# Kernel optimization log

Hardware: AMD Instinct MI355X
Metric: run time of the kernel (lower is better)

Reference implementation:

```python
import jax, jax.numpy as jnp
import numpy as np

# --- dimensions (match init_kwargs) ---
T, B = 64, 8            # time steps, batch
H, I, O, G = 512, 256, 8, 4   # hidden, input, output, attention groups
GS = I // G              # group size = 64 (equal groups)
E_H = int(0.8 * H)       # 409 excitatory hidden units
ZC = round(0.2 * H)      # 102 zeroed columns for h2o / attn masks
DT = 0.02
AX = DT / 0.1            # alpha_x = 0.2
AW = DT / 1.0            # alpha_w = 0.02

# --- static EI masks (constants of the architecture) ---
_sign_h = np.concatenate([np.ones(E_H), -np.ones(H - E_H)]).astype(np.float32)  # [H]
_m_h2h = np.tile(_sign_h, (H, 1)); np.fill_diagonal(_m_h2h, 0.0)                 # remove_diag
_exist = np.concatenate([np.ones(H - ZC), np.zeros(ZC)]).astype(np.float32)     # [H]
_m_attn = np.tile(_sign_h * _exist, (G, 1))   # attn: e_prop=0.8, zero_cols_prop=0.2
_m_h2o = np.tile(_exist, (O, 1))              # h2o: e_prop=1 (all +), zero last ZC cols
MASK_H2H = jnp.asarray(_m_h2h)
MASK_ATTN = jnp.asarray(_m_attn)
MASK_H2O = jnp.asarray(_m_h2o)


def setup_inputs() -> dict:
    key = jax.random.key(0)
    ks = jax.random.split(key, 8)
    x = jax.random.normal(ks[0], (T, B, I), dtype=jnp.float32)
    Rs = jax.random.uniform(ks[1], (T, B, 1), dtype=jnp.float32)
    # EILinear init: uniform(0, sqrt(1/(in - zero_cols))) * init_gain
    W_x2h = jax.random.uniform(ks[2], (H, I), dtype=jnp.float32, maxval=np.sqrt(1.0 / I)) * 0.5
    W_h2h = jax.random.uniform(ks[3], (H, H), dtype=jnp.float32, maxval=np.sqrt(1.0 / H))
    b_h2h = jnp.zeros((H,), jnp.float32)
    W_h2o = jax.random.uniform(ks[4], (O, H), dtype=jnp.float32, maxval=np.sqrt(1.0 / (H - ZC))) * 0.5
    W_attn = jax.random.uniform(ks[5], (G, H), dtype=jnp.float32, maxval=np.sqrt(1.0 / (H - ZC)))
    b_attn = jnp.zeros((G,), jnp.float32)
    kappa = jnp.full((6,), AW, dtype=jnp.float32)  # kappa_w init = alpha_w
    return {"x": x, "Rs": Rs, "W_x2h": W_x2h, "W_h2h": W_h2h, "b_h2h": b_h2h,
            "W_h2o": W_h2o, "W_attn": W_attn, "b_attn": b_attn, "kappa": kappa}


def reference(x, Rs, W_x2h, W_h2h, b_h2h, W_h2o, W_attn, b_attn, kappa):
    relu = jax.nn.relu
    Wx_pos = relu(W_x2h)                 # x2h mask is all ones (e_prop=1)
    Wh_pos = relu(W_h2h)
    eff_attn = relu(W_attn) * MASK_ATTN  # [G, H]
    Wx_floor = jax.lax.stop_gradient(Wx_pos)  # clamp bound (.detach())
    Wh_floor = jax.lax.stop_gradient(Wh_pos)

    def step(carry, inp):
        state, out, wx, wh = carry       # [B,H],[B,H],[B,H,I],[B,H,H]
        xt, Rt = inp                     # [B,I], [B,1]
        # attention gating over input groups
        aw = jax.nn.softmax(out @ eff_attn.T + b_attn, axis=-1)   # [B,G]
        af = jnp.repeat(aw, GS, axis=-1)                          # [B,I]
        xin = relu(xt) * af * G                                   # sigma_in = 0
        # plastic effective weights: (relu(W) + w) * mask
        eff_x = Wx_pos[None] + wx                                 # [B,H,I] (mask = ones)
        eff_h = (Wh_pos[None] + wh) * MASK_H2H[None]              # [B,H,H]
        total = (jnp.einsum('bhi,bi->bh', eff_x, xin)
                 + jnp.einsum('bhj,bj->bh', eff_h, out) + b_h2h)
        new_state = state * (1.0 - AX) + total * AX               # sigma_rec = 0
        new_out = jnp.tanh(relu(new_state))                       # retanh
        # Hebbian fast-weight updates (sigma_w = 0)
        R = Rt[:, :, None]                                        # [B,1,1]
        wx2 = wx * (1.0 - AW) + DT * R * (
            kappa[0] * xin[:, None, :]
            + kappa[1] * new_out[:, :, None]
            + kappa[2] * new_out[:, :, None] * xin[:, None, :])
        wx2 = jnp.maximum(wx2, -Wx_floor[None])
        wh2 = wh * (1.0 - AW) + DT * R * (
            kappa[3] * out[:, None, :]
            + kappa[4] * new_out[:, :, None]
            + kappa[5] * new_out[:, :, None] * out[:, None, :])
        wh2 = jnp.maximum(wh2, -Wh_floor[None])
        return (new_state, new_out, wx2, wh2), new_out

    init = (jnp.zeros((B, H), x.dtype), jnp.zeros((B, H), x.dtype),
            jnp.zeros((B, H, I), x.dtype), jnp.zeros((B, H, H), x.dtype))
    _, hs = jax.lax.scan(step, init, (x, Rs))                      # hs: [T,B,H]
    os = jnp.einsum('tbh,oh->tbo', hs, relu(W_h2o) * MASK_H2O)     # [T,B,O]
    return os, hs
```

## Files before the change

### kernel.cpp

```cpp
#include <hip/hip_runtime.h>

#define T_N 64
#define B_N 8
#define H_N 512
#define I_N 256
#define O_N 8
#define G_N 4

constexpr float DT_  = 0.02f;
constexpr float AX_  = 0.2f;
constexpr float AW_  = 0.02f;
constexpr float OMAW = 1.0f - AW_;

__device__ __forceinline__ float ldf_agent(const float* p) {
    return __hip_atomic_load(p, __ATOMIC_RELAXED, __HIP_MEMORY_SCOPE_AGENT);
}
__device__ __forceinline__ void stf_agent(float* p, float v) {
    __hip_atomic_store(p, v, __ATOMIC_RELAXED, __HIP_MEMORY_SCOPE_AGENT);
}
__device__ __forceinline__ unsigned ldu_agent(const unsigned* p) {
    return __hip_atomic_load(p, __ATOMIC_RELAXED, __HIP_MEMORY_SCOPE_AGENT);
}
__device__ __forceinline__ void stu_agent(unsigned* p, unsigned v) {
    __hip_atomic_store(p, v, __ATOMIC_RELAXED, __HIP_MEMORY_SCOPE_AGENT);
}

__device__ __forceinline__ float fast_tanh_pos(float x) {
    float ex = __expf(2.0f * x);
    return 1.0f - 2.0f / (ex + 1.0f);
}

__global__ __launch_bounds__(1024) void rnn_scan(
    const float* __restrict__ x, const float* __restrict__ Rs,
    const float* __restrict__ W_x2h, const float* __restrict__ W_h2h,
    const float* __restrict__ b_h2h, const float* __restrict__ W_h2o,
    const float* __restrict__ W_attn, const float* __restrict__ b_attn,
    const float* __restrict__ kappa, float* __restrict__ d_out,
    unsigned* __restrict__ flags,
    unsigned* __restrict__ barrier_cnt,
    float* __restrict__ vals)
{
    float* os = d_out;
    float* hs = d_out + T_N * B_N * O_N;

    __shared__ float s_out[H_N];

    const int tid  = threadIdx.x;
    const int wid  = tid >> 6;
    const int lane = tid & 63;
    const int bk   = blockIdx.x;
    const int b    = bk & 7;
    const int hg   = bk >> 3;
    const int h    = (hg << 4) | wid;
    const int c_d  = h >> 6;
    const int dl   = h & 63;

    float ea[G_N][7];
#pragma unroll
    for (int g = 0; g < G_N; ++g)
#pragma unroll
        for (int c = 0; c < 7; ++c) {
            int j = lane + 64 * c;
            float w = fmaxf(W_attn[g * H_N + j], 0.0f);
            float m = (j <= 408) ? 1.0f : ((j == 409) ? -1.0f : 0.0f);
            ea[g][c] = w * m;
        }

    float ex[4], bwx[4];
#pragma unroll
    for (int c = 0; c < 4; ++c) {
        ex[c]  = fmaxf(W_x2h[h * I_N + lane + 64 * c], 0.0f);
        bwx[c] = AW_ * ex[c];
    }
    float se[8], bwh[8];
#pragma unroll
    for (int c = 0; c < 8; ++c) {
        int j = lane + 64 * c;
        float s = (j <= 408) ? 1.0f : -1.0f;
        float w = fmaxf(W_h2h[h * H_N + j], 0.0f);
        se[c]  = (j == h) ? 0.0f : s * w;
        bwh[c] = AW_ * w;
    }
    const float bh = b_h2h[h];
    const float k0 = kappa[0], k1 = kappa[1], k2 = kappa[2];
    const float k3 = kappa[3], k4 = kappa[4], k5 = kappa[5];
    const float ba0 = b_attn[0], ba1 = b_attn[1], ba2 = b_attn[2], ba3 = b_attn[3];

    float st = 0.0f;

    float xv[4];
#pragma unroll
    for (int c = 0; c < 4; ++c) xv[c] = fmaxf(x[(size_t)b * I_N + lane + 64 * c], 0.0f);
    float Rcur = Rs[b];

    float outp[8];
#pragma unroll
    for (int c = 0; c < 8; ++c) outp[c] = 0.0f;

    for (int t = 0; t < T_N; ++t) {
        float red[9];
#pragma unroll
        for (int g = 0; g < G_N; ++g) {
            float l = 0.0f;
#pragma unroll
            for (int c = 0; c < 7; ++c) l = fmaf(outp[c], ea[g][c], l);
            red[g] = l;
        }
#pragma unroll
        for (int c = 0; c < 4; ++c) red[4 + c] = ex[c] * xv[c];
        {
            float a = 0.0f;
#pragma unroll
            for (int c = 0; c < 8; ++c) a = fmaf(se[c], outp[c], a);
            red[8] = a;
        }
#pragma unroll
        for (int off = 32; off >= 1; off >>= 1) {
#pragma unroll
            for (int k = 0; k < 9; ++k) red[k] += __shfl_xor(red[k], off, 64);
        }

        float e0 = __expf(red[0] + ba0), e1 = __expf(red[1] + ba1);
        float e2 = __expf(red[2] + ba2), e3 = __expf(red[3] + ba3);
        float inv = 4.0f / (e0 + e1 + e2 + e3);
        float aw0 = e0 * inv, aw1 = e1 * inv, aw2 = e2 * inv, aw3 = e3 * inv;

        float total = red[4] * aw0 + red[5] * aw1 + red[6] * aw2 + red[7] * aw3
                    + red[8] + bh;

        st = st * (1.0f - AX_) + total * AX_;
        float no = fast_tanh_pos(fmaxf(st, 0.0f));

        const int slot = t & 1;
        float* vrow = vals + ((size_t)slot * B_N + b) * H_N;
        if (lane == 0) {
            if (t + 1 < T_N) stf_agent(vrow + h, no);
            stf_agent(&hs[((size_t)t * B_N + b) * H_N + h], no);
        }

        if (t + 1 == T_N) break;

        const float* xr = x + ((size_t)(t + 1) * B_N + b) * I_N;
        float xvn[4];
#pragma unroll
        for (int c = 0; c < 4; ++c) xvn[c] = xr[lane + 64 * c];
        float Rn = Rs[(t + 1) * B_N + b];

        float xin[4] = { xv[0] * aw0, xv[1] * aw1, xv[2] * aw2, xv[3] * aw3 };
        float dr = DT_ * Rcur;
        float k1n = k1 * no, k2n = k2 * no, k4n = k4 * no, k5n = k5 * no;
#pragma unroll
        for (int c = 0; c < 4; ++c) {
            float hx = fmaf(k2n, xin[c], fmaf(k0, xin[c], k1n));
            ex[c] = fmaxf(fmaf(ex[c], OMAW, fmaf(dr, hx, bwx[c])), 0.0f);
        }
#pragma unroll
        for (int c = 0; c < 8; ++c) {
            float hh = fmaf(k5n, outp[c], fmaf(k3, outp[c], k4n));
            float a = se[c] * OMAW, p = fmaf(dr, hh, bwh[c]);
            float r;
            if (c <= 5)      r = fmaxf(a + p, 0.0f);
            else if (c == 7) r = fminf(a - p, 0.0f);
            else             r = (lane <= 24) ? fmaxf(a + p, 0.0f)
                                              : fminf(a - p, 0.0f);
            if (c == c_d && lane == dl) r = 0.0f;
            se[c] = r;
        }

        asm volatile("s_waitcnt vmcnt(0)" ::: "memory");
        __syncthreads();
        unsigned* fbase = flags + ((size_t)slot * B_N + b) * 32 * 32;
        if (tid == 0) stu_agent(fbase + hg * 32, (unsigned)(t + 1));

        if (wid == 0) {
            const unsigned want = (unsigned)(t + 1);
            bool ready = (lane >= 32);
            while (true) {
                if (!ready) ready = (ldu_agent(fbase + lane * 32) == want);
                if (__all(ready)) break;
                __builtin_amdgcn_s_sleep(1);
            }
            float tmp[8];
#pragma unroll
            for (int c = 0; c < 8; ++c) tmp[c] = ldf_agent(vrow + lane + 64 * c);
#pragma unroll
            for (int c = 0; c < 8; ++c) s_out[lane + 64 * c] = tmp[c];
        }
        __syncthreads();

#pragma unroll
        for (int c = 0; c < 8; ++c) outp[c] = s_out[lane + 64 * c];
#pragma unroll
        for (int c = 0; c < 4; ++c) xv[c] = fmaxf(xvn[c], 0.0f);
        Rcur = Rn;
    }

    unsigned* cnt = barrier_cnt + b * 32;
    asm volatile("s_waitcnt vmcnt(0)" ::: "memory");
    __syncthreads();
    if (tid == 0) {
        __hip_atomic_fetch_add(cnt, 1u, __ATOMIC_RELAXED, __HIP_MEMORY_SCOPE_AGENT);
        while (ldu_agent(cnt) < 32u) __builtin_amdgcn_s_sleep(2);
    }
    __syncthreads();

    {
        int v = (hg << 4) | wid;
        int t = v >> 3;
        int o = v & 7;
        const float* hrow = hs + ((size_t)t * B_N + b) * H_N;
        float acc = 0.0f;
#pragma unroll
        for (int c = 0; c < 7; ++c) {
            int j = lane + 64 * c;
            float w = fmaxf(W_h2o[o * H_N + j], 0.0f);
            if (j >= 410) w = 0.0f;
            acc = fmaf(ldf_agent(hrow + j), w, acc);
        }
#pragma unroll
        for (int off = 32; off >= 1; off >>= 1) acc += __shfl_xor(acc, off, 64);
        if (lane == 0) os[t * (B_N * O_N) + b * O_N + o] = acc;
    }
}

extern "C" void kernel_launch(void* const* d_in, const int* in_sizes, int n_in,
                              void* d_out, int out_size, void* d_ws, size_t ws_size,
                              hipStream_t stream) {
    (void)in_sizes; (void)n_in; (void)out_size; (void)ws_size;
    const float* x      = (const float*)d_in[0];
    const float* Rs     = (const float*)d_in[1];
    const float* W_x2h  = (const float*)d_in[2];
    const float* W_h2h  = (const float*)d_in[3];
    const float* b_h2h  = (const float*)d_in[4];
    const float* W_h2o  = (const float*)d_in[5];
    const float* W_attn = (const float*)d_in[6];
    const float* b_attn = (const float*)d_in[7];
    const float* kappa  = (const float*)d_in[8];
    float* out = (float*)d_out;

    unsigned* flags = (unsigned*)d_ws;
    unsigned* cnt   = (unsigned*)((char*)d_ws + 65536);
    float*    vals  = (float*)((char*)d_ws + 65536 + 1024);

    hipMemsetAsync(d_ws, 0, 65536 + 1024, stream);
    rnn_scan<<<dim3(256), dim3(1024), 0, stream>>>(
        x, Rs, W_x2h, W_h2h, b_h2h, W_h2o, W_attn, b_attn, kappa, out,
        flags, cnt, vals);
}
```

Before: 282.4 us.

## Replace flag-based block sync with sentinel-valued data polling and split output projection

Instead of each block publishing a separate flag after a block-wide barrier and then reloading values, the hs output is pre-filled with a NaN sentinel and wave 0 polls the hs row directly until every value is written. This removes the per-step __syncthreads plus waitcnt before signaling, the flag write, and the extra value buffer. The shared buffer becomes double-buffered. The final grid barrier and fused output projection are moved into a separate os_proj kernel. The exchange relies on tanh never producing the 0xFFFFFFFF bit pattern, and it adds a large memset plus a second launch.

Result: slower. 350.2 us (+24.0%).

```diff
diff --git a/kernel.cpp b/kernel.cpp
--- a/kernel.cpp
+++ b/kernel.cpp
@@ -12,17 +12,11 @@
 constexpr float AW_  = 0.02f;
 constexpr float OMAW = 1.0f - AW_;
 
-__device__ __forceinline__ float ldf_agent(const float* p) {
-    return __hip_atomic_load(p, __ATOMIC_RELAXED, __HIP_MEMORY_SCOPE_AGENT);
-}
 __device__ __forceinline__ void stf_agent(float* p, float v) {
     __hip_atomic_store(p, v, __ATOMIC_RELAXED, __HIP_MEMORY_SCOPE_AGENT);
 }
 __device__ __forceinline__ unsigned ldu_agent(const unsigned* p) {
     return __hip_atomic_load(p, __ATOMIC_RELAXED, __HIP_MEMORY_SCOPE_AGENT);
-}
-__device__ __forceinline__ void stu_agent(unsigned* p, unsigned v) {
-    __hip_atomic_store(p, v, __ATOMIC_RELAXED, __HIP_MEMORY_SCOPE_AGENT);
 }
 
 __device__ __forceinline__ float fast_tanh_pos(float x) {
@@ -30,20 +24,16 @@
     return 1.0f - 2.0f / (ex + 1.0f);
 }
 
+#define SENTINEL 0xFFFFFFFFu
+
 __global__ __launch_bounds__(1024) void rnn_scan(
     const float* __restrict__ x, const float* __restrict__ Rs,
     const float* __restrict__ W_x2h, const float* __restrict__ W_h2h,
-    const float* __restrict__ b_h2h, const float* __restrict__ W_h2o,
+    const float* __restrict__ b_h2h,
     const float* __restrict__ W_attn, const float* __restrict__ b_attn,
-    const float* __restrict__ kappa, float* __restrict__ d_out,
-    unsigned* __restrict__ flags,
-    unsigned* __restrict__ barrier_cnt,
-    float* __restrict__ vals)
+    const float* __restrict__ kappa, float* __restrict__ hs)
 {
-    float* os = d_out;
-    float* hs = d_out + T_N * B_N * O_N;
-
-    __shared__ float s_out[H_N];
+    __shared__ float s_out[2][H_N];
 
     const int tid  = threadIdx.x;
     const int wid  = tid >> 6;
@@ -131,12 +121,8 @@
         st = st * (1.0f - AX_) + total * AX_;
         float no = fast_tanh_pos(fmaxf(st, 0.0f));
 
-        const int slot = t & 1;
-        float* vrow = vals + ((size_t)slot * B_N + b) * H_N;
-        if (lane == 0) {
-            if (t + 1 < T_N) stf_agent(vrow + h, no);
-            stf_agent(&hs[((size_t)t * B_N + b) * H_N + h], no);
-        }
+        float* hrow = hs + ((size_t)t * B_N + b) * H_N;
+        if (lane == 0) stf_agent(hrow + h, no);
 
         if (t + 1 == T_N) break;
 
@@ -167,66 +153,66 @@
             se[c] = r;
         }
 
-        asm volatile("s_waitcnt vmcnt(0)" ::: "memory");
-        __syncthreads();
-        unsigned* fbase = flags + ((size_t)slot * B_N + b) * 32 * 32;
-        if (tid == 0) stu_agent(fbase + hg * 32, (unsigned)(t + 1));
-
         if (wid == 0) {
-            const unsigned want = (unsigned)(t + 1);
-            bool ready = (lane >= 32);
+            const unsigned* urow = (const unsigned*)hrow;
+            unsigned done = 0;
+            float v[8];
             while (true) {
-                if (!ready) ready = (ldu_agent(fbase + lane * 32) == want);
-                if (__all(ready)) break;
+#pragma unroll
+                for (int c = 0; c < 8; ++c) {
+                    if (!((done >> c) & 1u)) {
+                        unsigned u = ldu_agent(urow + lane + 64 * c);
+                        if (u != SENTINEL) {
+                            v[c] = __uint_as_float(u);
+                            done |= (1u << c);
+                        }
+                    }
+                }
+                if (__all(done == 0xFFu)) break;
                 __builtin_amdgcn_s_sleep(1);
             }
-            float tmp[8];
-#pragma unroll
-            for (int c = 0; c < 8; ++c) tmp[c] = ldf_agent(vrow + lane + 64 * c);
-#pragma unroll
-            for (int c = 0; c < 8; ++c) s_out[lane + 64 * c] = tmp[c];
+            float* sb = s_out[t & 1];
+#pragma unroll
+            for (int c = 0; c < 8; ++c) sb[lane + 64 * c] = v[c];
         }
         __syncthreads();
 
-#pragma unroll
-        for (int c = 0; c < 8; ++c) outp[c] = s_out[lane + 64 * c];
+        const float* sb = s_out[t & 1];
+#pragma unroll
+        for (int c = 0; c < 8; ++c) outp[c] = sb[lane + 64 * c];
 #pragma unroll
         for (int c = 0; c < 4; ++c) xv[c] = fmaxf(xvn[c], 0.0f);
         Rcur = Rn;
     }
-
-    unsigned* cnt = barrier_cnt + b * 32;
-    asm volatile("s_waitcnt vmcnt(0)" ::: "memory");
-    __syncthreads();
-    if (tid == 0) {
-        __hip_atomic_fetch_add(cnt, 1u, __ATOMIC_RELAXED, __HIP_MEMORY_SCOPE_AGENT);
-        while (ldu_agent(cnt) < 32u) __builtin_amdgcn_s_sleep(2);
-    }
-    __syncthreads();
-
-    {
-        int v = (hg << 4) | wid;
-        int t = v >> 3;
-        int o = v & 7;
-        const float* hrow = hs + ((size_t)t * B_N + b) * H_N;
-        float acc = 0.0f;
-#pragma unroll
-        for (int c = 0; c < 7; ++c) {
-            int j = lane + 64 * c;
-            float w = fmaxf(W_h2o[o * H_N + j], 0.0f);
-            if (j >= 410) w = 0.0f;
-            acc = fmaf(ldf_agent(hrow + j), w, acc);
-        }
-#pragma unroll
-        for (int off = 32; off >= 1; off >>= 1) acc += __shfl_xor(acc, off, 64);
-        if (lane == 0) os[t * (B_N * O_N) + b * O_N + o] = acc;
-    }
+}
+
+__global__ __launch_bounds__(512) void os_proj(
+    const float* __restrict__ hs, const float* __restrict__ W_h2o,
+    float* __restrict__ os)
+{
+    const int blk  = blockIdx.x;
+    const int t    = blk >> 3;
+    const int b    = blk & 7;
+    const int o    = threadIdx.x >> 6;
+    const int lane = threadIdx.x & 63;
+    const float* hrow = hs + ((size_t)t * B_N + b) * H_N;
+    float acc = 0.0f;
+#pragma unroll
+    for (int c = 0; c < 7; ++c) {
+        int j = lane + 64 * c;
+        float w = fmaxf(W_h2o[o * H_N + j], 0.0f);
+        if (j >= 410) w = 0.0f;
+        acc = fmaf(hrow[j], w, acc);
+    }
+#pragma unroll
+    for (int off = 32; off >= 1; off >>= 1) acc += __shfl_xor(acc, off, 64);
+    if (lane == 0) os[t * (B_N * O_N) + b * O_N + o] = acc;
 }
 
 extern "C" void kernel_launch(void* const* d_in, const int* in_sizes, int n_in,
                               void* d_out, int out_size, void* d_ws, size_t ws_size,
                               hipStream_t stream) {
-    (void)in_sizes; (void)n_in; (void)out_size; (void)ws_size;
+    (void)in_sizes; (void)n_in; (void)out_size; (void)d_ws; (void)ws_size;
     const float* x      = (const float*)d_in[0];
     const float* Rs     = (const float*)d_in[1];
     const float* W_x2h  = (const float*)d_in[2];
@@ -236,14 +222,11 @@
     const float* W_attn = (const float*)d_in[6];
     const float* b_attn = (const float*)d_in[7];
     const float* kappa  = (const float*)d_in[8];
-    float* out = (float*)d_out;
-
-    unsigned* flags = (unsigned*)d_ws;
-    unsigned* cnt   = (unsigned*)((char*)d_ws + 65536);
-    float*    vals  = (float*)((char*)d_ws + 65536 + 1024);
-
-    hipMemsetAsync(d_ws, 0, 65536 + 1024, stream);
+    float* os = (float*)d_out;
+    float* hs = (float*)d_out + T_N * B_N * O_N;
+
+    hipMemsetAsync(hs, 0xFF, (size_t)T_N * B_N * H_N * sizeof(float), stream);
     rnn_scan<<<dim3(256), dim3(1024), 0, stream>>>(
-        x, Rs, W_x2h, W_h2h, b_h2h, W_h2o, W_attn, b_attn, kappa, out,
-        flags, cnt, vals);
-}
+        x, Rs, W_x2h, W_h2h, b_h2h, W_attn, b_attn, kappa, hs);
+    os_proj<<<dim3(512), dim3(512), 0, stream>>>(hs, W_h2o, os);
+}
```
